# Performance work log

Measured on AMD Instinct MI355X. Metric: run time of the kernel, lower is better.

## Reference

```python
import jax, jax.numpy as jnp
import numpy as np

IMG = 512
C = 3
PS = 16
G = 32
B = 64
NH = IMG // PS
NW = IMG // PS
NP_ = NH * NW
P2 = PS * PS


def setup_inputs() -> dict:
    key = jax.random.key(0)
    k1, k2, k3, k4 = jax.random.split(key, 4)
    x = jax.random.normal(k1, (B, C, IMG, IMG), dtype=jnp.float32)
    # Conv2d(1, ps*ps, kernel=ps) default init ~ U(-1/ps, 1/ps); scale random normals similarly.
    obfuscation_weights = jax.random.normal(k2, (C, G, P2, P2), dtype=jnp.float32) / PS
    obfuscation_biases = jax.random.normal(k3, (C, G, P2), dtype=jnp.float32) / PS
    channel_permutation = jax.random.permutation(k4, jnp.arange(C, dtype=jnp.int32))
    return {
        "x": x,
        "obfuscation_weights": obfuscation_weights,
        "obfuscation_biases": obfuscation_biases,
        "channel_permutation": channel_permutation,
    }


def reference(x, obfuscation_weights, obfuscation_biases, channel_permutation):
    # x: (B, C, H, W) -> patches (B, C, N, ps*ps)
    x_patched = (
        x.reshape(B, C, NH, PS, NW, PS)
        .transpose(0, 1, 2, 4, 3, 5)
        .reshape(B, C, NP_, P2)
    )
    # group index per spatial patch: (row + col) % group_size
    ridx = jnp.arange(NH)[:, None]
    cidx = jnp.arange(NW)[None, :]
    group_map = ((ridx + cidx) % G).reshape(-1)  # (N,)
    sel_w = obfuscation_weights[:, group_map]  # (C, N, P2, P2)
    sel_b = obfuscation_biases[:, group_map]  # (C, N, P2)
    out = jnp.einsum("bcnp,cnpo->bcno", x_patched, sel_w) + sel_b
    # back to image layout
    out = (
        out.reshape(B, C, NH, NW, PS, PS)
        .transpose(0, 1, 2, 4, 3, 5)
        .reshape(B, C, IMG, IMG)
    )
    out = out[:, channel_permutation]
    return jnp.tanh(out)
```

## Files before the change

### kernel.cpp

```cpp
#include <hip/hip_runtime.h>

#define C_SZ   3
#define IMG_SZ 512
#define G_SZ   32

typedef short  short8 __attribute__((ext_vector_type(8)));
typedef float  f32x4  __attribute__((ext_vector_type(4)));
typedef unsigned short u16;
typedef u16    u16x8  __attribute__((ext_vector_type(8)));

__device__ __forceinline__ u16 f2bf(float f) {
    unsigned u = __float_as_uint(f);
    u += 0x7FFFu + ((u >> 16) & 1u);
    return (u16)(u >> 16);
}

__device__ __forceinline__ float tanh_fast(float v) {
    float e = __expf(2.f * v);
    return 1.f - 2.f * __builtin_amdgcn_rcpf(e + 1.f);
}

__global__ __launch_bounds__(256)
void prep_wt(const float* __restrict__ w, u16* __restrict__ wt) {
    const int cg = blockIdx.x;
    const int kb = blockIdx.y;
    __shared__ float T[32][260];
    const int tid = threadIdx.x;
    const float* wb = w + (size_t)cg * 65536 + (size_t)kb * 32 * 256;
    #pragma unroll
    for (int pass = 0; pass < 8; ++pass) {
        int q = pass * 256 + tid;
        int pl = q >> 6, o4 = (q & 63) * 4;
        float4 v = *reinterpret_cast<const float4*>(wb + (size_t)pl * 256 + o4);
        T[pl][o4 + 0] = v.x; T[pl][o4 + 1] = v.y;
        T[pl][o4 + 2] = v.z; T[pl][o4 + 3] = v.w;
    }
    __syncthreads();
    u16* dst = wt + ((size_t)cg * 8 + kb) * 8192;
    #pragma unroll
    for (int h0 = 0; h0 < 4; ++h0) {
        int h = h0 * 256 + tid;
        int kg = h >> 8, n = h & 255;
        u16x8 v;
        #pragma unroll
        for (int e = 0; e < 8; ++e) v[e] = f2bf(T[kg * 8 + e][n]);
        *reinterpret_cast<u16x8*>(dst + (size_t)kg * 2048 + n * 8) = v;
    }
}

__global__ __launch_bounds__(256, 3)
void obf_mfma(const float* __restrict__ x,
              const u16*  __restrict__ wt,
              const float* __restrict__ bias,
              const int*  __restrict__ perm,
              float* __restrict__ out)
{
    const int bid  = blockIdx.x;
    const int sbid = (bid & 7) * 384 + (bid >> 3);
    const int mtile = sbid & 31;
    const int cg    = sbid >> 5;
    const int c = cg >> 5, g = cg & 31;
    const int tid  = threadIdx.x;
    const int lane = tid & 63, wv = tid >> 6;

    __shared__ u16 As[2][64][40];

    f32x4 acc[4][4] = {};

    int cp = 0;
    #pragma unroll
    for (int i = 0; i < C_SZ; ++i) if (perm[i] == c) cp = i;

    const float* a_src[2];
    int a_off[2];
    #pragma unroll
    for (int pass = 0; pass < 2; ++pass) {
        int q    = pass * 256 + tid;
        int ml   = q >> 3, half = (q >> 2) & 1, f4 = q & 3;
        int mg   = mtile * 64 + ml;
        int b    = mg >> 5, nh = mg & 31, nw = (g - nh) & 31;
        a_src[pass] = x + (((size_t)(b * C_SZ + c) * IMG_SZ + nh * 16 + half) * IMG_SZ
                           + nw * 16 + f4 * 4);
        a_off[pass] = ml * 40 + half * 16 + f4 * 4;
    }
    const int r = lane & 15, kg = lane >> 4;
    const u16* bsrc = wt + (size_t)cg * 65536 + kg * 2048 + ((size_t)(wv * 64 + r)) * 8;

    f32x4 av[2];
    av[0] = *reinterpret_cast<const f32x4*>(a_src[0]);
    av[1] = *reinterpret_cast<const f32x4*>(a_src[1]);
    short8 bfrag[4];
    #pragma unroll
    for (int ni = 0; ni < 4; ++ni)
        bfrag[ni] = *reinterpret_cast<const short8*>(bsrc + ni * 128);
    #pragma unroll
    for (int pass = 0; pass < 2; ++pass) {
        u16* d = &As[0][0][0] + a_off[pass];
        d[0] = f2bf(av[pass][0]); d[1] = f2bf(av[pass][1]);
        d[2] = f2bf(av[pass][2]); d[3] = f2bf(av[pass][3]);
    }
    __syncthreads();

    const int koff = kg * 8;
    #pragma unroll
    for (int ks = 0; ks < 8; ++ks) {
        f32x4 an[2];
        short8 bn[4];
        if (ks < 7) {
            an[0] = *reinterpret_cast<const f32x4*>(a_src[0] + (size_t)(ks + 1) * 2 * IMG_SZ);
            an[1] = *reinterpret_cast<const f32x4*>(a_src[1] + (size_t)(ks + 1) * 2 * IMG_SZ);
            #pragma unroll
            for (int ni = 0; ni < 4; ++ni)
                bn[ni] = *reinterpret_cast<const short8*>(bsrc + (ks + 1) * 8192 + ni * 128);
        }
        const u16* abase = &As[ks & 1][0][0];
        short8 a[4];
        #pragma unroll
        for (int mi = 0; mi < 4; ++mi)
            a[mi] = *reinterpret_cast<const short8*>(abase + (mi * 16 + r) * 40 + koff);
        #pragma unroll
        for (int mi = 0; mi < 4; ++mi)
            #pragma unroll
            for (int ni = 0; ni < 4; ++ni)
                acc[mi][ni] = __builtin_amdgcn_mfma_f32_16x16x32_bf16(
                    a[mi], bfrag[ni], acc[mi][ni], 0, 0, 0);
        if (ks < 7) {
            u16* d0 = &As[(ks & 1) ^ 1][0][0];
            #pragma unroll
            for (int pass = 0; pass < 2; ++pass) {
                u16* d = d0 + a_off[pass];
                d[0] = f2bf(an[pass][0]); d[1] = f2bf(an[pass][1]);
                d[2] = f2bf(an[pass][2]); d[3] = f2bf(an[pass][3]);
            }
            #pragma unroll
            for (int ni = 0; ni < 4; ++ni) bfrag[ni] = bn[ni];
        }
        __syncthreads();
    }

    const int cc = lane & 15;
    float bs[4];
    #pragma unroll
    for (int ni = 0; ni < 4; ++ni)
        bs[ni] = bias[(size_t)cg * 256 + wv * 64 + ni * 16 + cc];

    #pragma unroll
    for (int mi = 0; mi < 4; ++mi) {
        #pragma unroll
        for (int reg = 0; reg < 4; ++reg) {
            const int ml = mi * 16 + (lane >> 4) * 4 + reg;
            const int mg = mtile * 64 + ml;
            const int b  = mg >> 5, nh = mg & 31, nw = (g - nh) & 31;
            float* orow = out + ((size_t)(b * C_SZ + cp) * IMG_SZ + nh * 16) * IMG_SZ
                              + nw * 16 + cc;
            #pragma unroll
            for (int ni = 0; ni < 4; ++ni) {
                const int rp = wv * 4 + ni;
                orow[(size_t)rp * IMG_SZ] = tanh_fast(acc[mi][ni][reg] + bs[ni]);
            }
        }
    }
}

extern "C" void kernel_launch(void* const* d_in, const int* in_sizes, int n_in,
                              void* d_out, int out_size, void* d_ws, size_t ws_size,
                              hipStream_t stream) {
    const float* x    = (const float*)d_in[0];
    const float* w    = (const float*)d_in[1];
    const float* bias = (const float*)d_in[2];
    const int*   perm = (const int*)d_in[3];
    float* out = (float*)d_out;
    u16*   wt  = (u16*)d_ws;

    dim3 pgrid(C_SZ * G_SZ, 8, 1);
    prep_wt<<<pgrid, 256, 0, stream>>>(w, wt);

    obf_mfma<<<3072, 256, 0, stream>>>(x, wt, bias, perm, out);
}
```

Before: 149.8 us.

## Load activation fragments straight from global memory, dropping LDS staging and barriers

Each wave now reads its bf16 A fragments for the MFMA directly from global memory into registers and converts them there. This replaces the shared-memory double buffer and the per-k-step __syncthreads. The aim is to remove the LDS write/read traffic and barrier stalls. In exchange, all four waves re-read the same activation data, relying on L1/L2 to serve the repeats. Access is less coalesced, with 32-byte pieces from 16 scattered patches per instruction, and the explicit next-step prefetch is gone.

Result: slower. 220.4 us (+47.1%).

```diff
diff --git a/kernel.cpp b/kernel.cpp
--- a/kernel.cpp
+++ b/kernel.cpp
@@ -62,80 +62,51 @@
     const int c = cg >> 5, g = cg & 31;
     const int tid  = threadIdx.x;
     const int lane = tid & 63, wv = tid >> 6;
-
-    __shared__ u16 As[2][64][40];
-
-    f32x4 acc[4][4] = {};
+    const int r = lane & 15, kg = lane >> 4;
 
     int cp = 0;
     #pragma unroll
     for (int i = 0; i < C_SZ; ++i) if (perm[i] == c) cp = i;
 
-    const float* a_src[2];
-    int a_off[2];
+    const float* asrc[4];
     #pragma unroll
-    for (int pass = 0; pass < 2; ++pass) {
-        int q    = pass * 256 + tid;
-        int ml   = q >> 3, half = (q >> 2) & 1, f4 = q & 3;
-        int mg   = mtile * 64 + ml;
-        int b    = mg >> 5, nh = mg & 31, nw = (g - nh) & 31;
-        a_src[pass] = x + (((size_t)(b * C_SZ + c) * IMG_SZ + nh * 16 + half) * IMG_SZ
-                           + nw * 16 + f4 * 4);
-        a_off[pass] = ml * 40 + half * 16 + f4 * 4;
+    for (int mi = 0; mi < 4; ++mi) {
+        int mg = mtile * 64 + mi * 16 + r;
+        int b  = mg >> 5, nh = mg & 31, nw = (g - nh) & 31;
+        asrc[mi] = x + (((size_t)(b * C_SZ + c) * IMG_SZ + nh * 16 + (kg >> 1)) * IMG_SZ
+                        + nw * 16 + (kg & 1) * 8);
     }
-    const int r = lane & 15, kg = lane >> 4;
-    const u16* bsrc = wt + (size_t)cg * 65536 + kg * 2048 + ((size_t)(wv * 64 + r)) * 8;
+    const u16* bsrc = wt + (size_t)cg * 65536 + kg * 2048 + (size_t)(wv * 64 + r) * 8;
 
-    f32x4 av[2];
-    av[0] = *reinterpret_cast<const f32x4*>(a_src[0]);
-    av[1] = *reinterpret_cast<const f32x4*>(a_src[1]);
-    short8 bfrag[4];
-    #pragma unroll
-    for (int ni = 0; ni < 4; ++ni)
-        bfrag[ni] = *reinterpret_cast<const short8*>(bsrc + ni * 128);
-    #pragma unroll
-    for (int pass = 0; pass < 2; ++pass) {
-        u16* d = &As[0][0][0] + a_off[pass];
-        d[0] = f2bf(av[pass][0]); d[1] = f2bf(av[pass][1]);
-        d[2] = f2bf(av[pass][2]); d[3] = f2bf(av[pass][3]);
-    }
-    __syncthreads();
+    f32x4 acc[4][4] = {};
 
-    const int koff = kg * 8;
     #pragma unroll
     for (int ks = 0; ks < 8; ++ks) {
-        f32x4 an[2];
-        short8 bn[4];
-        if (ks < 7) {
-            an[0] = *reinterpret_cast<const f32x4*>(a_src[0] + (size_t)(ks + 1) * 2 * IMG_SZ);
-            an[1] = *reinterpret_cast<const f32x4*>(a_src[1] + (size_t)(ks + 1) * 2 * IMG_SZ);
+        f32x4 alo[4], ahi[4];
+        #pragma unroll
+        for (int mi = 0; mi < 4; ++mi) {
+            alo[mi] = *reinterpret_cast<const f32x4*>(asrc[mi] + ks * 1024);
+            ahi[mi] = *reinterpret_cast<const f32x4*>(asrc[mi] + ks * 1024 + 4);
+        }
+        short8 bf[4];
+        #pragma unroll
+        for (int ni = 0; ni < 4; ++ni)
+            bf[ni] = *reinterpret_cast<const short8*>(bsrc + ks * 8192 + ni * 128);
+        short8 af[4];
+        #pragma unroll
+        for (int mi = 0; mi < 4; ++mi) {
             #pragma unroll
-            for (int ni = 0; ni < 4; ++ni)
-                bn[ni] = *reinterpret_cast<const short8*>(bsrc + (ks + 1) * 8192 + ni * 128);
+            for (int e = 0; e < 4; ++e) {
+                af[mi][e]     = (short)f2bf(alo[mi][e]);
+                af[mi][4 + e] = (short)f2bf(ahi[mi][e]);
+            }
         }
-        const u16* abase = &As[ks & 1][0][0];
-        short8 a[4];
-        #pragma unroll
-        for (int mi = 0; mi < 4; ++mi)
-            a[mi] = *reinterpret_cast<const short8*>(abase + (mi * 16 + r) * 40 + koff);
         #pragma unroll
         for (int mi = 0; mi < 4; ++mi)
             #pragma unroll
             for (int ni = 0; ni < 4; ++ni)
                 acc[mi][ni] = __builtin_amdgcn_mfma_f32_16x16x32_bf16(
-                    a[mi], bfrag[ni], acc[mi][ni], 0, 0, 0);
-        if (ks < 7) {
-            u16* d0 = &As[(ks & 1) ^ 1][0][0];
-            #pragma unroll
-            for (int pass = 0; pass < 2; ++pass) {
-                u16* d = d0 + a_off[pass];
-                d[0] = f2bf(an[pass][0]); d[1] = f2bf(an[pass][1]);
-                d[2] = f2bf(an[pass][2]); d[3] = f2bf(an[pass][3]);
-            }
-            #pragma unroll
-            for (int ni = 0; ni < 4; ++ni) bfrag[ni] = bn[ni];
-        }
-        __syncthreads();
+                    af[mi], bf[ni], acc[mi][ni], 0, 0, 0);
     }
 
     const int cc = lane & 15;
@@ -148,7 +119,7 @@
     for (int mi = 0; mi < 4; ++mi) {
         #pragma unroll
         for (int reg = 0; reg < 4; ++reg) {
-            const int ml = mi * 16 + (lane >> 4) * 4 + reg;
+            const int ml = mi * 16 + kg * 4 + reg;
             const int mg = mtile * 64 + ml;
             const int b  = mg >> 5, nh = mg & 31, nw = (g - nh) & 31;
             float* orow = out + ((size_t)(b * C_SZ + cp) * IMG_SZ + nh * 16) * IMG_SZ
```
